# Performance work log

Hardware: AMD Instinct MI355X
Metric: run time of the kernel (lower is better)

Reference implementation:

```python
import jax, jax.numpy as jnp
import numpy as np

N, D, K, ITERS = 500000, 64, 256, 10


def setup_inputs() -> dict:
    key = jax.random.key(0)
    k1, k2 = jax.random.split(key)
    x = jax.random.normal(k1, (N, D), dtype=jnp.float32)
    init_idx = jax.random.randint(k2, (K,), 0, N, dtype=jnp.int32)
    return {"x": x, "init_idx": init_idx, "n_clusters": K, "n_iters": ITERS}


def _lloyd_step(x, x_sq, centroids):
    dists = x_sq[:, None] - 2.0 * (x @ centroids.T) + jnp.sum(centroids * centroids, axis=1)[None, :]
    assign = jnp.argmin(dists, axis=1)                       # [N]
    sums = jax.ops.segment_sum(x, assign, num_segments=centroids.shape[0])   # [K, D]
    counts = jax.ops.segment_sum(jnp.ones((x.shape[0],), x.dtype), assign,
                                 num_segments=centroids.shape[0])            # [K]
    new_c = sums / jnp.maximum(counts, 1.0)[:, None]
    # empty clusters keep their previous centroid (sklearn relocates; carry-over is the standard Lloyd fallback)
    return jnp.where(counts[:, None] > 0, new_c, centroids)


def reference(x, init_idx, n_clusters, n_iters):
    # original: x.detach() -> no gradient flows through k-means
    x = jax.lax.stop_gradient(x)
    x_sq = jnp.sum(x * x, axis=1)  # [N], reused every iteration
    centroids0 = x[init_idx]       # [K, D] random-point init

    def body(c, _):
        return _lloyd_step(x, x_sq, c), None

    centroids, _ = jax.lax.scan(body, centroids0, None, length=n_iters)
    return centroids  # cluster_centers_ [K, D]
```

## Files before the change

kernel.cpp:

```cpp
#include <hip/hip_runtime.h>


#define D 64
#define K 256
#define ITERS 10
#define BLOCK 1024
#define NB_MAX 256
#define EPS 2e-2f
#define SPAD 66
#define PART_STRIDE (K * D + K)
#define SMEM_BYTES (32768 * 2 + (256 + 256 * SPAD + 256) * 4)

typedef __attribute__((ext_vector_type(8))) short bf16x8;
typedef __attribute__((ext_vector_type(4))) float f32x4;
typedef __attribute__((ext_vector_type(4))) short short4v;

__device__ __forceinline__ unsigned short f2bf(float f) {
    unsigned u = __builtin_bit_cast(unsigned, f);
    u = u + 0x7FFFu + ((u >> 16) & 1u);
    return (unsigned short)(u >> 16);
}
__device__ __forceinline__ float bf2f(unsigned short h) {
    unsigned u = ((unsigned)h) << 16;
    return __builtin_bit_cast(float, u);
}

__global__ void init_gather(const float* __restrict__ x,
                            const int* __restrict__ idx,
                            float* __restrict__ cent,
                            float* __restrict__ csq) {
    int k = blockIdx.x;
    int d = threadIdx.x;
    float v = x[(size_t)idx[k] * D + d];
    cent[k * D + d] = v;
    float s = v * v;
    #pragma unroll
    for (int off = 32; off > 0; off >>= 1) s += __shfl_down(s, off);
    if (d == 0) csq[k] = s;
}

__device__ __forceinline__ int resolve_bk(
        const f32x4 (&acc)[16], const float* __restrict__ s_csq,
        const float* __restrict__ cent, const float* __restrict__ xr,
        int g4) {
    float gmin = 3.4e38f;
    int gidx = 0;
    #pragma unroll
    for (int t = 0; t < 16; ++t) {
        f32x4 q = *(const f32x4*)&s_csq[t * 16 + (g4 << 2)];
        #pragma unroll
        for (int r = 0; r < 4; ++r) {
            float sc = acc[t][r] + q[r];
            int m = t * 16 + (g4 << 2) + r;
            if (sc < gmin) { gmin = sc; gidx = m; }
        }
    }
    #pragma unroll
    for (int off = 16; off <= 32; off <<= 1) {
        float so = __shfl_xor(gmin, off);
        int io = __shfl_xor(gidx, off);
        if (so < gmin || (so == gmin && io < gidx)) { gmin = so; gidx = io; }
    }
    unsigned long long cmask = 0;
    #pragma unroll
    for (int t = 0; t < 16; ++t) {
        f32x4 q = *(const f32x4*)&s_csq[t * 16 + (g4 << 2)];
        #pragma unroll
        for (int r = 0; r < 4; ++r) {
            float sc = acc[t][r] + q[r];
            if (sc <= gmin + EPS) cmask |= 1ull << (t * 4 + r);
        }
    }
    int nb_ = __popcll(cmask);
    nb_ += __shfl_xor(nb_, 16);
    nb_ += __shfl_xor(nb_, 32);

    int bk = gidx;
    if (__any(nb_ >= 2)) {
        float xsq = 0.0f;
        #pragma unroll
        for (int d = 0; d < D; ++d) xsq += xr[d] * xr[d];
        float eb = 3.4e38f;
        int em = 0x7fffffff;
        unsigned long long mm = cmask;
        while (mm) {
            int b = __ffsll((unsigned long long)mm) - 1;
            mm &= mm - 1;
            int m = ((b >> 2) << 4) + (g4 << 2) + (b & 3);
            const float* cr = cent + m * D;
            float dot = 0.0f;
            #pragma unroll
            for (int d4 = 0; d4 < D; d4 += 4) {
                float4 c4 = *(const float4*)(cr + d4);
                dot += c4.x * xr[d4 + 0];
                dot += c4.y * xr[d4 + 1];
                dot += c4.z * xr[d4 + 2];
                dot += c4.w * xr[d4 + 3];
            }
            float es = xsq - 2.0f * dot + s_csq[m];
            if (es < eb || (es == eb && m < em)) { eb = es; em = m; }
        }
        #pragma unroll
        for (int off = 16; off <= 32; off <<= 1) {
            float so = __shfl_xor(eb, off);
            int io = __shfl_xor(em, off);
            if (so < eb || (so == eb && io < em)) { eb = so; em = io; }
        }
        bk = em;
    }
    return bk;
}

__global__ __launch_bounds__(BLOCK, 4) void assign_mfma(
        const float* __restrict__ x,
        const float* __restrict__ cent,
        const float* __restrict__ csq_g,
        float* __restrict__ parts,
        int N, int ppb) {
    extern __shared__ char smem[];
    short* chi = (short*)smem;
    short* clo = chi + 16384;
    float* s_csq = (float*)(clo + 16384);
    float* s_sums = s_csq + 256;
    float* s_cnt = s_sums + 256 * SPAD;

    const int tid = threadIdx.x;

    for (int i = tid; i < (K * D) / 4; i += BLOCK) {
        float4 c4 = ((const float4*)cent)[i];
        int elem = i * 4;
        int m = elem >> 6;
        int k0 = elem & 63;
        int g = k0 >> 3, e0 = k0 & 7;
        float cv[4] = {c4.x, c4.y, c4.z, c4.w};
        short4v hv, lv;
        #pragma unroll
        for (int j = 0; j < 4; ++j) {
            float v = -2.0f * cv[j];
            unsigned short h = f2bf(v);
            hv[j] = (short)h;
            lv[j] = (short)f2bf(v - bf2f(h));
        }
        int dst = (g * 256 + m) * 8 + e0;
        *(short4v*)&chi[dst] = hv;
        *(short4v*)&clo[dst] = lv;
    }
    if (tid < K) s_csq[tid] = csq_g[tid];
    for (int i = tid; i < 256 * SPAD; i += BLOCK) s_sums[i] = 0.0f;
    if (tid < K) s_cnt[tid] = 0.0f;
    __syncthreads();

    const int wv = tid >> 6;
    const int lane = tid & 63;
    const int c15 = lane & 15;
    const int g4 = lane >> 4;

    const int base = blockIdx.x * ppb;
    int lim = base + ppb;
    if (lim > N) lim = N;
    const int ngroups = (lim > base) ? ((lim - base + 15) >> 4) : 0;

    #pragma unroll 1
    for (int g0 = wv; g0 < ngroups; g0 += 16) {
        int prow = base + g0 * 16 + c15;
        const bool vA = prow < lim;
        const float* xr = x + (size_t)(vA ? prow : (lim - 1)) * D;

        float xf[16];
        bf16x8 bh[2], bl[2];
        #pragma unroll
        for (int s = 0; s < 2; ++s) {
            const float4* pa = (const float4*)(xr + s * 32 + g4 * 8);
            float4 a0 = pa[0], a1 = pa[1];
            xf[s * 8 + 0] = a0.x; xf[s * 8 + 1] = a0.y;
            xf[s * 8 + 2] = a0.z; xf[s * 8 + 3] = a0.w;
            xf[s * 8 + 4] = a1.x; xf[s * 8 + 5] = a1.y;
            xf[s * 8 + 6] = a1.z; xf[s * 8 + 7] = a1.w;
        }
        #pragma unroll
        for (int s = 0; s < 2; ++s) {
            #pragma unroll
            for (int e = 0; e < 8; ++e) {
                float va = xf[s * 8 + e];
                unsigned short ha = f2bf(va);
                bh[s][e] = (short)ha;
                bl[s][e] = (short)f2bf(va - bf2f(ha));
            }
        }

        f32x4 acc[16];
        #pragma unroll
        for (int t = 0; t < 16; ++t) {
            f32x4 z = {0.f, 0.f, 0.f, 0.f};
            acc[t] = z;
            #pragma unroll
            for (int s = 0; s < 2; ++s) {
                int ai = (((s * 4 + g4) * 256) + t * 16 + c15) * 8;
                bf16x8 ah = *(const bf16x8*)&chi[ai];
                bf16x8 al = *(const bf16x8*)&clo[ai];
                acc[t] = __builtin_amdgcn_mfma_f32_16x16x32_bf16(ah, bh[s], acc[t], 0, 0, 0);
                acc[t] = __builtin_amdgcn_mfma_f32_16x16x32_bf16(ah, bl[s], acc[t], 0, 0, 0);
                acc[t] = __builtin_amdgcn_mfma_f32_16x16x32_bf16(al, bh[s], acc[t], 0, 0, 0);
            }
        }

        int bk = resolve_bk(acc, s_csq, cent, xr, g4);
        if (vA) {
            #pragma unroll
            for (int s = 0; s < 2; ++s) {
                #pragma unroll
                for (int e = 0; e < 8; ++e)
                    atomicAdd(&s_sums[bk * SPAD + s * 32 + g4 * 8 + e],
                              xf[s * 8 + e]);
            }
            if (g4 == 0) atomicAdd(&s_cnt[bk], 1.0f);
        }
    }

    __syncthreads();
    float* part = parts + (size_t)blockIdx.x * PART_STRIDE;
    for (int i = tid; i < K * D; i += BLOCK) {
        int k = i >> 6, d = i & 63;
        part[i] = s_sums[k * SPAD + d];
    }
    if (tid < K) part[K * D + tid] = s_cnt[tid];
}

__global__ void finalize2(float* __restrict__ cent,
                          const float* __restrict__ parts,
                          float* __restrict__ csq_g,
                          int nb) {
    __shared__ float tmp[4][64];
    __shared__ float tcnt[4];
    int k = blockIdx.x;
    int sl = threadIdx.x >> 6;
    int d = threadIdx.x & 63;
    float s = 0.0f, c = 0.0f;
    for (int b = sl; b < nb; b += 4) {
        const float* pb = parts + (size_t)b * PART_STRIDE;
        s += pb[k * D + d];
        c += pb[K * D + k];
    }
    tmp[sl][d] = s;
    if (d == 0) tcnt[sl] = c;
    __syncthreads();
    if (sl == 0) {
        float st = tmp[0][d] + tmp[1][d] + tmp[2][d] + tmp[3][d];
        float ct = tcnt[0] + tcnt[1] + tcnt[2] + tcnt[3];
        float oldc = cent[k * D + d];
        float nc = (ct > 0.0f) ? (st / ct) : oldc;
        cent[k * D + d] = nc;
        float v = nc * nc;
        #pragma unroll
        for (int off = 32; off > 0; off >>= 1) v += __shfl_down(v, off);
        if (d == 0) csq_g[k] = v;
    }
}

extern "C" void kernel_launch(void* const* d_in, const int* in_sizes, int n_in,
                              void* d_out, int out_size, void* d_ws, size_t ws_size,
                              hipStream_t stream) {
    const float* x = (const float*)d_in[0];
    const int* init_idx = (const int*)d_in[1];

    int N = in_sizes[0] / D;

    float* cent = (float*)d_out;

    int nb = NB_MAX;
    size_t need = ((size_t)NB_MAX * PART_STRIDE + K) * sizeof(float);
    if (ws_size < need) {
        size_t avail = (ws_size > (size_t)K * sizeof(float))
                           ? ws_size - (size_t)K * sizeof(float) : 0;
        nb = (int)(avail / (PART_STRIDE * sizeof(float)));
        if (nb < 1) nb = 1;
    }
    float* parts = (float*)d_ws;
    float* csq = parts + (size_t)nb * PART_STRIDE;

    hipFuncSetAttribute(reinterpret_cast<const void*>(assign_mfma),
                        hipFuncAttributeMaxDynamicSharedMemorySize, SMEM_BYTES);

    init_gather<<<dim3(K), dim3(64), 0, stream>>>(x, init_idx, cent, csq);

    int ppb = (N + nb - 1) / nb;
    for (int it = 0; it < ITERS; ++it) {
        assign_mfma<<<dim3(nb), dim3(BLOCK), SMEM_BYTES, stream>>>(
            x, cent, csq, parts, N, ppb);
        finalize2<<<dim3(K), dim3(256), 0, stream>>>(cent, parts, csq, nb);
    }
}
```

Before: 2.388 ms.

## Double-buffer x loads, stagger centroid tiles per wave, use packed bf16 convert

The x rows for the next group are prefetched into a second register buffer while the current group runs its MFMAs and argmin, and the first load is issued before the centroid staging in shared memory. Each wave starts its centroid tile loop at a different offset to spread LDS bank and port contention. The hi/lo bf16 split now uses the hardware packed convert instruction, and wave priority is raised around the MFMA block. The extra register buffer may raise register pressure at 1024-thread blocks.

```diff
diff --git a/kernel.cpp b/kernel.cpp
--- a/kernel.cpp
+++ b/kernel.cpp
@@ -14,6 +14,7 @@
 typedef __attribute__((ext_vector_type(8))) short bf16x8;
 typedef __attribute__((ext_vector_type(4))) float f32x4;
 typedef __attribute__((ext_vector_type(4))) short short4v;
+typedef __attribute__((ext_vector_type(4))) unsigned int u32x4;
 
 __device__ __forceinline__ unsigned short f2bf(float f) {
     unsigned u = __builtin_bit_cast(unsigned, f);
@@ -23,6 +24,11 @@
 __device__ __forceinline__ float bf2f(unsigned short h) {
     unsigned u = ((unsigned)h) << 16;
     return __builtin_bit_cast(float, u);
+}
+__device__ __forceinline__ unsigned cvt_pk(float a, float b) {
+    unsigned r;
+    asm("v_cvt_pk_bf16_f32 %0, %1, %2" : "=v"(r) : "v"(a), "v"(b));
+    return r;
 }
 
 __global__ void init_gather(const float* __restrict__ x,
@@ -39,19 +45,63 @@
     if (d == 0) csq[k] = s;
 }
 
-__device__ __forceinline__ int resolve_bk(
-        const f32x4 (&acc)[16], const float* __restrict__ s_csq,
-        const float* __restrict__ cent, const float* __restrict__ xr,
-        int g4) {
+__device__ __forceinline__ void process_group(
+        const float (&xf)[16], int g, int base, int lim,
+        int c15, int g4, int wv,
+        const short* __restrict__ chi, const short* __restrict__ clo,
+        const float* __restrict__ s_csq, float* __restrict__ s_sums,
+        float* __restrict__ s_cnt,
+        const float* __restrict__ x, const float* __restrict__ cent) {
+    int prow = base + g * 16 + c15;
+    const bool vA = prow < lim;
+    const float* xr = x + (size_t)(vA ? prow : (lim - 1)) * D;
+
+    bf16x8 bh[2], bl[2];
+    #pragma unroll
+    for (int s = 0; s < 2; ++s) {
+        u32x4 h4, l4;
+        #pragma unroll
+        for (int e2 = 0; e2 < 4; ++e2) {
+            float a = xf[s * 8 + 2 * e2], b = xf[s * 8 + 2 * e2 + 1];
+            unsigned hw = cvt_pk(a, b);
+            h4[e2] = hw;
+            float ha = bf2f((unsigned short)(hw & 0xFFFFu));
+            float hb = bf2f((unsigned short)(hw >> 16));
+            l4[e2] = cvt_pk(a - ha, b - hb);
+        }
+        bh[s] = __builtin_bit_cast(bf16x8, h4);
+        bl[s] = __builtin_bit_cast(bf16x8, l4);
+    }
+
+    f32x4 acc[16];
+    __builtin_amdgcn_s_setprio(1);
+    #pragma unroll
+    for (int tt = 0; tt < 16; ++tt) {
+        int ta = (tt + wv) & 15;
+        f32x4 z = {0.f, 0.f, 0.f, 0.f};
+        acc[tt] = z;
+        #pragma unroll
+        for (int s = 0; s < 2; ++s) {
+            int ai = (((s * 4 + g4) * 256) + ta * 16 + c15) * 8;
+            bf16x8 ah = *(const bf16x8*)&chi[ai];
+            bf16x8 al = *(const bf16x8*)&clo[ai];
+            acc[tt] = __builtin_amdgcn_mfma_f32_16x16x32_bf16(ah, bh[s], acc[tt], 0, 0, 0);
+            acc[tt] = __builtin_amdgcn_mfma_f32_16x16x32_bf16(ah, bl[s], acc[tt], 0, 0, 0);
+            acc[tt] = __builtin_amdgcn_mfma_f32_16x16x32_bf16(al, bh[s], acc[tt], 0, 0, 0);
+        }
+    }
+    __builtin_amdgcn_s_setprio(0);
+
     float gmin = 3.4e38f;
     int gidx = 0;
     #pragma unroll
-    for (int t = 0; t < 16; ++t) {
-        f32x4 q = *(const f32x4*)&s_csq[t * 16 + (g4 << 2)];
+    for (int tt = 0; tt < 16; ++tt) {
+        int ta = (tt + wv) & 15;
+        f32x4 q = *(const f32x4*)&s_csq[ta * 16 + (g4 << 2)];
         #pragma unroll
         for (int r = 0; r < 4; ++r) {
-            float sc = acc[t][r] + q[r];
-            int m = t * 16 + (g4 << 2) + r;
+            float sc = acc[tt][r] + q[r];
+            int m = ta * 16 + (g4 << 2) + r;
             if (sc < gmin) { gmin = sc; gidx = m; }
         }
     }
@@ -63,12 +113,13 @@
     }
     unsigned long long cmask = 0;
     #pragma unroll
-    for (int t = 0; t < 16; ++t) {
-        f32x4 q = *(const f32x4*)&s_csq[t * 16 + (g4 << 2)];
+    for (int tt = 0; tt < 16; ++tt) {
+        int ta = (tt + wv) & 15;
+        f32x4 q = *(const f32x4*)&s_csq[ta * 16 + (g4 << 2)];
         #pragma unroll
         for (int r = 0; r < 4; ++r) {
-            float sc = acc[t][r] + q[r];
-            if (sc <= gmin + EPS) cmask |= 1ull << (t * 4 + r);
+            float sc = acc[tt][r] + q[r];
+            if (sc <= gmin + EPS) cmask |= 1ull << (ta * 4 + r);
         }
     }
     int nb_ = __popcll(cmask);
@@ -108,7 +159,17 @@
         }
         bk = em;
     }
-    return bk;
+
+    if (vA) {
+        #pragma unroll
+        for (int s = 0; s < 2; ++s) {
+            #pragma unroll
+            for (int e = 0; e < 8; ++e)
+                atomicAdd(&s_sums[bk * SPAD + s * 32 + g4 * 8 + e],
+                          xf[s * 8 + e]);
+        }
+        if (g4 == 0) atomicAdd(&s_cnt[bk], 1.0f);
+    }
 }
 
 __global__ __launch_bounds__(BLOCK, 4) void assign_mfma(
@@ -125,6 +186,33 @@
     float* s_cnt = s_sums + 256 * SPAD;
 
     const int tid = threadIdx.x;
+    const int wv = tid >> 6;
+    const int lane = tid & 63;
+    const int c15 = lane & 15;
+    const int g4 = lane >> 4;
+
+    const int base = blockIdx.x * ppb;
+    int lim = base + ppb;
+    if (lim > N) lim = N;
+    const int ngroups = (lim > base) ? ((lim - base + 15) >> 4) : 0;
+
+#define LOADX(dst, grp)                                                     \
+    {                                                                       \
+        int pr_ = base + (grp) * 16 + c15;                                  \
+        const float* xp_ =                                                  \
+            x + (size_t)((pr_ < lim) ? pr_ : (lim - 1)) * D + g4 * 8;       \
+        float4 t0_ = *(const float4*)(xp_);                                 \
+        float4 t1_ = *(const float4*)(xp_ + 4);                             \
+        float4 t2_ = *(const float4*)(xp_ + 32);                            \
+        float4 t3_ = *(const float4*)(xp_ + 36);                            \
+        dst[0] = t0_.x;  dst[1] = t0_.y;  dst[2] = t0_.z;  dst[3] = t0_.w;  \
+        dst[4] = t1_.x;  dst[5] = t1_.y;  dst[6] = t1_.z;  dst[7] = t1_.w;  \
+        dst[8] = t2_.x;  dst[9] = t2_.y;  dst[10] = t2_.z; dst[11] = t2_.w; \
+        dst[12] = t3_.x; dst[13] = t3_.y; dst[14] = t3_.z; dst[15] = t3_.w; \
+    }
+
+    float xfA[16], xfB[16];
+    if (wv < ngroups) LOADX(xfA, wv);
 
     for (int i = tid; i < (K * D) / 4; i += BLOCK) {
         float4 c4 = ((const float4*)cent)[i];
@@ -150,72 +238,21 @@
     if (tid < K) s_cnt[tid] = 0.0f;
     __syncthreads();
 
-    const int wv = tid >> 6;
-    const int lane = tid & 63;
-    const int c15 = lane & 15;
-    const int g4 = lane >> 4;
-
-    const int base = blockIdx.x * ppb;
-    int lim = base + ppb;
-    if (lim > N) lim = N;
-    const int ngroups = (lim > base) ? ((lim - base + 15) >> 4) : 0;
-
     #pragma unroll 1
-    for (int g0 = wv; g0 < ngroups; g0 += 16) {
-        int prow = base + g0 * 16 + c15;
-        const bool vA = prow < lim;
-        const float* xr = x + (size_t)(vA ? prow : (lim - 1)) * D;
-
-        float xf[16];
-        bf16x8 bh[2], bl[2];
-        #pragma unroll
-        for (int s = 0; s < 2; ++s) {
-            const float4* pa = (const float4*)(xr + s * 32 + g4 * 8);
-            float4 a0 = pa[0], a1 = pa[1];
-            xf[s * 8 + 0] = a0.x; xf[s * 8 + 1] = a0.y;
-            xf[s * 8 + 2] = a0.z; xf[s * 8 + 3] = a0.w;
-            xf[s * 8 + 4] = a1.x; xf[s * 8 + 5] = a1.y;
-            xf[s * 8 + 6] = a1.z; xf[s * 8 + 7] = a1.w;
-        }
-        #pragma unroll
-        for (int s = 0; s < 2; ++s) {
-            #pragma unroll
-            for (int e = 0; e < 8; ++e) {
-                float va = xf[s * 8 + e];
-                unsigned short ha = f2bf(va);
-                bh[s][e] = (short)ha;
-                bl[s][e] = (short)f2bf(va - bf2f(ha));
-            }
-        }
-
-        f32x4 acc[16];
-        #pragma unroll
-        for (int t = 0; t < 16; ++t) {
-            f32x4 z = {0.f, 0.f, 0.f, 0.f};
-            acc[t] = z;
-            #pragma unroll
-            for (int s = 0; s < 2; ++s) {
-                int ai = (((s * 4 + g4) * 256) + t * 16 + c15) * 8;
-                bf16x8 ah = *(const bf16x8*)&chi[ai];
-                bf16x8 al = *(const bf16x8*)&clo[ai];
-                acc[t] = __builtin_amdgcn_mfma_f32_16x16x32_bf16(ah, bh[s], acc[t], 0, 0, 0);
-                acc[t] = __builtin_amdgcn_mfma_f32_16x16x32_bf16(ah, bl[s], acc[t], 0, 0, 0);
-                acc[t] = __builtin_amdgcn_mfma_f32_16x16x32_bf16(al, bh[s], acc[t], 0, 0, 0);
-            }
-        }
-
-        int bk = resolve_bk(acc, s_csq, cent, xr, g4);
-        if (vA) {
-            #pragma unroll
-            for (int s = 0; s < 2; ++s) {
-                #pragma unroll
-                for (int e = 0; e < 8; ++e)
-                    atomicAdd(&s_sums[bk * SPAD + s * 32 + g4 * 8 + e],
-                              xf[s * 8 + e]);
-            }
-            if (g4 == 0) atomicAdd(&s_cnt[bk], 1.0f);
-        }
-    }
+    for (int g = wv; g < ngroups; g += 32) {
+        int gB = g + 16;
+        bool hB = gB < ngroups;
+        if (hB) LOADX(xfB, gB);
+        process_group(xfA, g, base, lim, c15, g4, wv,
+                      chi, clo, s_csq, s_sums, s_cnt, x, cent);
+        if (hB) {
+            int gC = gB + 16;
+            if (gC < ngroups) LOADX(xfA, gC);
+            process_group(xfB, gB, base, lim, c15, g4, wv,
+                          chi, clo, s_csq, s_sums, s_cnt, x, cent);
+        }
+    }
+#undef LOADX
 
     __syncthreads();
     float* part = parts + (size_t)blockIdx.x * PART_STRIDE;
```

Measured after the change: 6.563 ms. +174.8%, slower.
